# Kernel tuning notes

Hardware: AMD Instinct MI355X
Metric: run time of the kernel (lower is better)

## Reference

```python
import jax, jax.numpy as jnp
import numpy as np

B, T, D, H = 8192, 128, 16, 32
EPS = 1e-5  # BatchNorm1d default eps (eval mode, running stats)


def setup_inputs() -> dict:
    key = jax.random.key(0)
    ks = iter(jax.random.split(key, 64))

    def nrm(shape, s=0.1):
        return jax.random.normal(next(ks), shape, jnp.float32) * s

    inp = {}
    inp["S"] = nrm((B, T, D), 1.0)
    inp["g_S"] = nrm((B, T), 1.0)
    inp["times"] = jnp.linspace(0.0, 1.0, T, dtype=jnp.float32)
    inp["payoff_T"] = nrm((B,), 1.0)
    inp["delta_T"] = nrm((B, D), 1.0)
    # init_hidden: uniform(-0.1, 0.1), shape [num_layers=2, B, H]
    inp["h_price0"] = jax.random.uniform(next(ks), (2, B, H), jnp.float32, -0.1, 0.1)
    inp["h_delta0"] = jax.random.uniform(next(ks), (2, B, H), jnp.float32, -0.1, 0.1)
    # params for price net (prefix p_, out_dim=1) and delta net (prefix d_, out_dim=D)
    for pfx, out_dim in (("p", 1), ("d", D)):
        inp[pfx + "_Wih0"] = nrm((3 * H, 2 * D))
        inp[pfx + "_Whh0"] = nrm((3 * H, H))
        inp[pfx + "_bih0"] = nrm((3 * H,))
        inp[pfx + "_bhh0"] = nrm((3 * H,))
        inp[pfx + "_Wih1"] = nrm((3 * H, H))
        inp[pfx + "_Whh1"] = nrm((3 * H, H))
        inp[pfx + "_bih1"] = nrm((3 * H,))
        inp[pfx + "_bhh1"] = nrm((3 * H,))
        inp[pfx + "_embW"] = nrm((H, H))
        inp[pfx + "_embB"] = nrm((H,))
        inp[pfx + "_bng"] = jnp.ones((H,), jnp.float32)
        inp[pfx + "_bnb"] = jnp.zeros((H,), jnp.float32)
        inp[pfx + "_bnm"] = nrm((H,))
        inp[pfx + "_bnv"] = jax.random.uniform(next(ks), (H,), jnp.float32, 0.5, 1.5)
        inp[pfx + "_outW"] = nrm((out_dim, H))
        inp[pfx + "_outB"] = nrm((out_dim,))
    return inp


def _gru_cell(x, h, Wih, Whh, bih, bhh):
    # PyTorch GRU cell, gate order (r, z, n)
    gi = x @ Wih.T + bih
    gh = h @ Whh.T + bhh
    ir, iz, inn = jnp.split(gi, 3, axis=-1)
    hr, hz, hn = jnp.split(gh, 3, axis=-1)
    r = jax.nn.sigmoid(ir + hr)
    z = jax.nn.sigmoid(iz + hz)
    n = jnp.tanh(inn + r * hn)
    return (1.0 - z) * n + z * h


def _head(y, Wemb, bemb, g, b, m, v, Wout, bout, sig):
    # Linear -> BatchNorm1d (eval, running stats) -> SiLU -> Linear [-> Sigmoid]
    e = y @ Wemb.T + bemb
    e = (e - m) * jax.lax.rsqrt(v + EPS) * g + b
    e = e * jax.nn.sigmoid(e)  # SiLU
    o = e @ Wout.T + bout
    return jax.nn.sigmoid(o) if sig else o


def reference(S, g_S, times, payoff_T, delta_T, h_price0, h_delta0,
              p_Wih0, p_Whh0, p_bih0, p_bhh0, p_Wih1, p_Whh1, p_bih1, p_bhh1,
              p_embW, p_embB, p_bng, p_bnb, p_bnm, p_bnv, p_outW, p_outB,
              d_Wih0, d_Whh0, d_bih0, d_bhh0, d_Wih1, d_Whh1, d_bih1, d_bhh1,
              d_embW, d_embB, d_bng, d_bnb, d_bnm, d_bnv, d_outW, d_outB):
    # X = cat([S, g_S expanded to d]) -> [B, T, 2D]
    gS = jnp.broadcast_to(g_S[..., None], S.shape)
    X = jnp.concatenate([S, gS], axis=-1)
    Xr = jnp.swapaxes(X, 0, 1)[::-1]  # [T, B, 2D], time reversed (loop goes t=T-1..0)

    def step(carry, xt):
        hp0, hp1, hd0, hd1 = carry
        hp0 = _gru_cell(xt, hp0, p_Wih0, p_Whh0, p_bih0, p_bhh0)
        hp1 = _gru_cell(hp0, hp1, p_Wih1, p_Whh1, p_bih1, p_bhh1)
        hd0 = _gru_cell(xt, hd0, d_Wih0, d_Whh0, d_bih0, d_bhh0)
        hd1 = _gru_cell(hd0, hd1, d_Wih1, d_Whh1, d_bih1, d_bhh1)
        return (hp0, hp1, hd0, hd1), (hp1, hd1)

    carry0 = (h_price0[0], h_price0[1], h_delta0[0], h_delta0[1])
    _, (Yp, Yd) = jax.lax.scan(step, carry0, Xr)
    # flip time back to forward order: outputs were collected for t=T-1..0
    Yp = jnp.swapaxes(Yp[::-1], 0, 1)  # [B, T, H]
    Yd = jnp.swapaxes(Yd[::-1], 0, 1)  # [B, T, H]
    prices = _head(Yp, p_embW, p_embB, p_bng, p_bnb, p_bnm, p_bnv, p_outW, p_outB, False)  # [B,T,1]
    deltas = _head(Yd, d_embW, d_embB, d_bng, d_bnb, d_bnm, d_bnv, d_outW, d_outB, True)   # [B,T,D]
    return (prices, deltas)
```

## Files before the change

### kernel.cpp

```cpp
#include <hip/hip_runtime.h>
#include <hip/hip_bf16.h>
#include <stdint.h>

#define DI __device__ __forceinline__

typedef float f32x4 __attribute__((ext_vector_type(4)));
typedef short bf16x8 __attribute__((ext_vector_type(8)));

constexpr int BB = 8192, TT = 128, DD = 16, HH = 32;
constexpr float kEPS = 1e-5f;
constexpr float kLOG2E = 1.44269504088896340736f;

DI float rcpf_(float x) { return __builtin_amdgcn_rcpf(x); }
DI float exp2f_(float x) { return __builtin_amdgcn_exp2f(x); }
DI float sigm(float x) { return rcpf_(1.0f + exp2f_(-kLOG2E * x)); }

DI uint32_t cvtpk(float lo, float hi) {
  uint32_t r;
  asm("v_cvt_pk_bf16_f32 %0, %1, %2" : "=v"(r) : "v"(lo), "v"(hi));
  return r;
}

DI f32x4 mfma_(bf16x8 a, bf16x8 b, f32x4 c) {
  return __builtin_amdgcn_mfma_f32_16x16x32_bf16(a, b, c, 0, 0, 0);
}

union U4 { uint4 q; bf16x8 v; uint32_t u[4]; };

__global__ void prep_net(const float* Wih0, const float* Whh0,
                         const float* bih0, const float* bhh0,
                         const float* Wih1, const float* Whh1,
                         const float* bih1, const float* bhh1,
                         const float* embW, const float* embB,
                         const float* bng, const float* bnb,
                         const float* bnm, const float* bnv,
                         const float* outW, const float* outB,
                         int outDim, uint8_t* wsbase) {
  int tid = threadIdx.x;
  uint16_t* W = (uint16_t*)wsbase;
  float* bias = (float*)(wsbase + 27648);
  auto cvt = [](float f) -> uint16_t {
    union { float f; uint32_t u; } v; v.f = f;
    uint32_t u = v.u;
    return (uint16_t)((u + 0x7FFF + ((u >> 16) & 1)) >> 16);
  };
  for (int idx = tid; idx < 27 * 64; idx += 256) {
    int tile = idx >> 6, l = idx & 63, cc = l & 15, gg = l >> 4;
    uint16_t* dst = W + (size_t)idx * 8;
    if (tile < 24) {
      const float* mats[4] = {Wih0, Whh0, Wih1, Whh1};
      const float* src = mats[tile / 6];
      int sub = tile % 6;
      int row = sub * 16 + cc;
      float sc = (sub < 4) ? -kLOG2E : 2.0f * kLOG2E;
#pragma unroll
      for (int j = 0; j < 8; ++j) {
        int k = (j < 4) ? 4 * gg + j : 16 + 4 * gg + (j - 4);
        dst[j] = cvt(src[row * 32 + k] * sc);
      }
    } else if (tile < 26) {
      int row = (tile - 24) * 16 + cc;
      float a = bng[row] * rsqrtf(bnv[row] + kEPS);
#pragma unroll
      for (int j = 0; j < 8; ++j) {
        int k = (j < 4) ? 4 * gg + j : 16 + 4 * gg + (j - 4);
        dst[j] = cvt(embW[row * 32 + k] * a);
      }
    } else {
      int rrow = (cc < outDim) ? cc : 0;
      float sc = (cc < outDim) ? 1.0f : 0.0f;
#pragma unroll
      for (int j = 0; j < 8; ++j) {
        int k = (j < 4) ? 4 * gg + j : 16 + 4 * gg + (j - 4);
        dst[j] = cvt(outW[rrow * 32 + k] * sc);
      }
    }
  }
  for (int idx = tid; idx < 304; idx += 256) {
    int tile = idx >> 4, n = idx & 15;
    float v;
    if (tile < 8) {
      if (tile < 4)      v = (bih0[tile * 16 + n] + bhh0[tile * 16 + n]) * (-kLOG2E);
      else if (tile < 6) v = bih0[64 + (tile - 4) * 16 + n] * (2.0f * kLOG2E);
      else               v = bhh0[64 + (tile - 6) * 16 + n] * (2.0f * kLOG2E);
    } else if (tile < 16) {
      int tt = tile - 8;
      if (tt < 4)        v = (bih1[tt * 16 + n] + bhh1[tt * 16 + n]) * (-kLOG2E);
      else if (tt < 6)   v = bih1[64 + (tt - 4) * 16 + n] * (2.0f * kLOG2E);
      else               v = bhh1[64 + (tt - 6) * 16 + n] * (2.0f * kLOG2E);
    } else if (tile < 18) {
      int nn = (tile - 16) * 16 + n;
      float a = bng[nn] * rsqrtf(bnv[nn] + kEPS);
      v = a * (embB[nn] - bnm[nn]) + bnb[nn];
    } else {
      v = (n < outDim) ? outB[n] : 0.0f;
    }
    bias[idx] = v;
  }
}

__global__ __launch_bounds__(128, 2) void rnn_fused(
    const float* __restrict__ S, const float* __restrict__ gS,
    const float* __restrict__ hp0, const float* __restrict__ hd0,
    const uint8_t* __restrict__ ws, float* __restrict__ out) {
  const int tid = threadIdx.x, lane = tid & 63, wid = tid >> 6;
  const int net = blockIdx.x & 1;
  const int b0 = (blockIdx.x >> 1) * 16;
  const int c = lane & 15, g = lane >> 4;

  const uint16_t* W = (const uint16_t*)(ws + net * 32768);
  const float* bias = (const float*)(ws + net * 32768 + 27648);
  const float* hsrc = net ? hd0 : hp0;

  __shared__ uint4 ring0[8][64];
  __shared__ volatile int flags[2];
  if (tid < 2) flags[tid] = 0;
  __syncthreads();

  auto waitGE = [&](int idx, int target) {
    if (flags[idx] >= target) return;
    do { __builtin_amdgcn_s_sleep(1); } while (flags[idx] < target);
  };

  auto packB = [&](const float (&v)[8]) -> bf16x8 {
    U4 t;
    t.u[0] = cvtpk(v[0], v[1]); t.u[1] = cvtpk(v[2], v[3]);
    t.u[2] = cvtpk(v[4], v[5]); t.u[3] = cvtpk(v[6], v[7]);
    return t.v;
  };

  auto gruStep = [&](const bf16x8 (&Wi)[6], const bf16x8 (&Wh)[6],
                     const f32x4 (&Bb)[8], bf16x8 xf, bf16x8 hf,
                     float (&hC)[8]) {
    f32x4 r0 = mfma_(Wi[0], xf, Bb[0]); r0 = mfma_(Wh[0], hf, r0);
    f32x4 r1 = mfma_(Wi[1], xf, Bb[1]); r1 = mfma_(Wh[1], hf, r1);
    f32x4 z0 = mfma_(Wi[2], xf, Bb[2]); z0 = mfma_(Wh[2], hf, z0);
    f32x4 z1 = mfma_(Wi[3], xf, Bb[3]); z1 = mfma_(Wh[3], hf, z1);
    f32x4 ni0 = mfma_(Wi[4], xf, Bb[4]);
    f32x4 ni1 = mfma_(Wi[5], xf, Bb[5]);
    f32x4 nh0 = mfma_(Wh[4], hf, Bb[6]);
    f32x4 nh1 = mfma_(Wh[5], hf, Bb[7]);
#pragma unroll
    for (int r = 0; r < 4; ++r) {
      float rg0 = rcpf_(1.0f + exp2f_(r0[r]));
      float rg1 = rcpf_(1.0f + exp2f_(r1[r]));
      float w0 = ni0[r] + rg0 * nh0[r];
      float w1 = ni1[r] + rg1 * nh1[r];
      float En0 = exp2f_(w0), En1 = exp2f_(w1);
      float Ez0 = exp2f_(z0[r]), Ez1 = exp2f_(z1[r]);
      float hv0 = hC[r], hv1 = hC[4 + r];
      float num0 = (hv0 - Ez0) + En0 * (hv0 + Ez0);
      float num1 = (hv1 - Ez1) + En1 * (hv1 + Ez1);
      float den0 = (1.0f + En0) * (1.0f + Ez0);
      float den1 = (1.0f + En1) * (1.0f + Ez1);
      hC[r]     = num0 * rcpf_(den0);
      hC[4 + r] = num1 * rcpf_(den1);
    }
  };

  auto loadState = [&](const float* row, float (&hC)[8]) -> bf16x8 {
    f32x4 a = *(const f32x4*)(row + 4 * g);
    f32x4 b = *(const f32x4*)(row + 16 + 4 * g);
#pragma unroll
    for (int r = 0; r < 4; ++r) { hC[r] = a[r]; hC[4 + r] = b[r]; }
    U4 t;
    t.u[0] = cvtpk(a[0], a[1]); t.u[1] = cvtpk(a[2], a[3]);
    t.u[2] = cvtpk(b[0], b[1]); t.u[3] = cvtpk(b[2], b[3]);
    return t.v;
  };

  if (wid == 0) {
    bf16x8 Wi[6], Wh[6];
#pragma unroll
    for (int t = 0; t < 6; ++t) {
      Wi[t] = *(const bf16x8*)(W + ((0 + t) * 64 + lane) * 8);
      Wh[t] = *(const bf16x8*)(W + ((6 + t) * 64 + lane) * 8);
    }
    f32x4 Bb[8];
#pragma unroll
    for (int t = 0; t < 8; ++t)
      Bb[t] = *(const f32x4*)(bias + t * 16 + 4 * g);

    float h0C[8];
    bf16x8 h0B = loadState(hsrc + (size_t)(b0 + c) * HH, h0C);

    auto mkX = [&](f32x4 sv, float gsv) -> bf16x8 {
      uint32_t pkg = cvtpk(gsv, gsv);
      U4 t;
      t.u[0] = cvtpk(sv[0], sv[1]);
      t.u[1] = cvtpk(sv[2], sv[3]);
      t.u[2] = pkg;
      t.u[3] = pkg;
      return t.v;
    };

    const float* Sbase  = S  + (size_t)(b0 + c) * TT * DD + 4 * g;
    const float* gSbase = gS + (size_t)(b0 + c) * TT;

    f32x4 sv0 = *(const f32x4*)(Sbase + (size_t)(TT - 1) * DD);
    float gv0 = gSbase[TT - 1];
    f32x4 sv1 = *(const f32x4*)(Sbase + (size_t)(TT - 2) * DD);
    float gv1 = gSbase[TT - 2];

#pragma unroll 2
    for (int i = 0; i < TT; ++i) {
      int tn = TT - 3 - i; if (tn < 0) tn = 0;
      f32x4 svn = *(const f32x4*)(Sbase + (size_t)tn * DD);
      float gvn = gSbase[tn];

      bf16x8 xB = mkX(sv0, gv0);
      gruStep(Wi, Wh, Bb, xB, h0B, h0C);
      h0B = packB(h0C);

      if (i >= 8 && (i & 3) == 0) waitGE(1, i - 4);
      asm volatile("" ::: "memory");
      { U4 u; u.v = h0B; ring0[i & 7][lane] = u.q; }
      if ((i & 3) == 3) {
        asm volatile("s_waitcnt lgkmcnt(0)" ::: "memory");
        if (lane == 0) flags[0] = i + 1;
      }

      sv0 = sv1; gv0 = gv1;
      sv1 = svn; gv1 = gvn;
    }
  } else {
    bf16x8 Wi[6], Wh[6], We0, We1, Wo;
#pragma unroll
    for (int t = 0; t < 6; ++t) {
      Wi[t] = *(const bf16x8*)(W + ((12 + t) * 64 + lane) * 8);
      Wh[t] = *(const bf16x8*)(W + ((18 + t) * 64 + lane) * 8);
    }
    We0 = *(const bf16x8*)(W + (24 * 64 + lane) * 8);
    We1 = *(const bf16x8*)(W + (25 * 64 + lane) * 8);
    Wo  = *(const bf16x8*)(W + (26 * 64 + lane) * 8);
    f32x4 Bb[8];
#pragma unroll
    for (int t = 0; t < 8; ++t)
      Bb[t] = *(const f32x4*)(bias + (8 + t) * 16 + 4 * g);
    const f32x4 Be0 = *(const f32x4*)(bias + 16 * 16 + 4 * g);
    const f32x4 Be1 = *(const f32x4*)(bias + 17 * 16 + 4 * g);
    const f32x4 Bo  = *(const f32x4*)(bias + 18 * 16 + 4 * g);

    float h1C[8];
    bf16x8 h1B = loadState(hsrc + ((size_t)BB + b0 + c) * HH, h1C);

    auto head = [&](bf16x8 h1f, int th) {
      f32x4 e0 = mfma_(We0, h1f, Be0);
      f32x4 e1 = mfma_(We1, h1f, Be1);
      float es[8];
#pragma unroll
      for (int r = 0; r < 4; ++r) {
        float a = e0[r], b = e1[r];
        es[r]     = a * sigm(a);
        es[4 + r] = b * sigm(b);
      }
      bf16x8 ef = packB(es);
      f32x4 o = mfma_(Wo, ef, Bo);
      if (net == 0) {
        if (lane < 16) out[(size_t)(b0 + c) * TT + th] = o[0];
      } else {
        f32x4 so;
#pragma unroll
        for (int r = 0; r < 4; ++r) so[r] = sigm(o[r]);
        *(f32x4*)(out + (size_t)BB * TT +
                  ((size_t)(b0 + c) * TT + th) * DD + 4 * g) = so;
      }
    };

#pragma unroll 1
    for (int i = 0; i < TT; ++i) {
      if ((i & 3) == 0) waitGE(0, i + 4);
      asm volatile("" ::: "memory");
      U4 u; u.q = ring0[i & 7][lane];
      asm volatile("s_waitcnt lgkmcnt(0)" ::: "memory");
      if ((i & 3) == 3 && lane == 0) flags[1] = i + 1;

      bf16x8 h1prev = h1B;
      gruStep(Wi, Wh, Bb, u.v, h1B, h1C);
      if (i > 0) head(h1prev, TT - i);
      h1B = packB(h1C);
    }
    head(h1B, 0);
  }
}

extern "C" void kernel_launch(void* const* d_in, const int* in_sizes, int n_in,
                              void* d_out, int out_size, void* d_ws,
                              size_t ws_size, hipStream_t stream) {
  const float* S   = (const float*)d_in[0];
  const float* gS  = (const float*)d_in[1];
  const float* hp0 = (const float*)d_in[5];
  const float* hd0 = (const float*)d_in[6];
  uint8_t* ws = (uint8_t*)d_ws;

  prep_net<<<1, 256, 0, stream>>>(
      (const float*)d_in[7],  (const float*)d_in[8],  (const float*)d_in[9],
      (const float*)d_in[10], (const float*)d_in[11], (const float*)d_in[12],
      (const float*)d_in[13], (const float*)d_in[14], (const float*)d_in[15],
      (const float*)d_in[16], (const float*)d_in[17], (const float*)d_in[18],
      (const float*)d_in[19], (const float*)d_in[20], (const float*)d_in[21],
      (const float*)d_in[22], 1, ws);
  prep_net<<<1, 256, 0, stream>>>(
      (const float*)d_in[23], (const float*)d_in[24], (const float*)d_in[25],
      (const float*)d_in[26], (const float*)d_in[27], (const float*)d_in[28],
      (const float*)d_in[29], (const float*)d_in[30], (const float*)d_in[31],
      (const float*)d_in[32], (const float*)d_in[33], (const float*)d_in[34],
      (const float*)d_in[35], (const float*)d_in[36], (const float*)d_in[37],
      (const float*)d_in[38], 16, ws + 32768);

  rnn_fused<<<dim3((BB / 16) * 2), dim3(128), 0, stream>>>(S, gS, hp0, hd0,
                                                           ws, (float*)d_out);
}
```

Before: 151.4 us.

## Split layer-1 GRU and output head into separate warps with second ring

Adds a third wavefront per block so that the layer-0 GRU, the layer-1 GRU and the embedding/output head each run on their own wave, connected by LDS ring buffers and flag handshakes. The head work moves off the layer-1 recurrence critical path. Each wave now processes two timesteps per loop iteration with one flag update, which cuts synchronisation frequency. The cost is more threads per block, an extra ring buffer and tighter occupancy, since launch bounds change to 192 threads with 3 blocks per CU.

```diff
diff --git a/kernel.cpp b/kernel.cpp
--- a/kernel.cpp
+++ b/kernel.cpp
@@ -99,7 +99,7 @@
   }
 }
 
-__global__ __launch_bounds__(128, 2) void rnn_fused(
+__global__ __launch_bounds__(192, 3) void rnn_fused(
     const float* __restrict__ S, const float* __restrict__ gS,
     const float* __restrict__ hp0, const float* __restrict__ hd0,
     const uint8_t* __restrict__ ws, float* __restrict__ out) {
@@ -113,8 +113,9 @@
   const float* hsrc = net ? hd0 : hp0;
 
   __shared__ uint4 ring0[8][64];
-  __shared__ volatile int flags[2];
-  if (tid < 2) flags[tid] = 0;
+  __shared__ uint4 ring1[8][64];
+  __shared__ volatile int flags[4];
+  if (tid < 4) flags[tid] = 0;
   __syncthreads();
 
   auto waitGE = [&](int idx, int target) {
@@ -196,53 +197,87 @@
 
     const float* Sbase  = S  + (size_t)(b0 + c) * TT * DD + 4 * g;
     const float* gSbase = gS + (size_t)(b0 + c) * TT;
-
-    f32x4 sv0 = *(const f32x4*)(Sbase + (size_t)(TT - 1) * DD);
-    float gv0 = gSbase[TT - 1];
-    f32x4 sv1 = *(const f32x4*)(Sbase + (size_t)(TT - 2) * DD);
-    float gv1 = gSbase[TT - 2];
-
-#pragma unroll 2
-    for (int i = 0; i < TT; ++i) {
-      int tn = TT - 3 - i; if (tn < 0) tn = 0;
-      f32x4 svn = *(const f32x4*)(Sbase + (size_t)tn * DD);
-      float gvn = gSbase[tn];
-
-      bf16x8 xB = mkX(sv0, gv0);
-      gruStep(Wi, Wh, Bb, xB, h0B, h0C);
+    auto loadX = [&](int t, f32x4& a, float& gv) {
+      a = *(const f32x4*)(Sbase + (size_t)t * DD); gv = gSbase[t];
+    };
+
+    f32x4 ca0, ca1, na0, na1;
+    float cg0, cg1, ng0, ng1;
+    loadX(TT - 1, ca0, cg0);
+    loadX(TT - 2, ca1, cg1);
+
+#pragma unroll 1
+    for (int ip = 0; ip < TT / 2; ++ip) {
+      int tn0 = TT - 3 - 2 * ip; if (tn0 < 0) tn0 = 0;
+      int tn1 = TT - 4 - 2 * ip; if (tn1 < 0) tn1 = 0;
+      loadX(tn0, na0, ng0);
+      loadX(tn1, na1, ng1);
+
+      bf16x8 x0 = mkX(ca0, cg0);
+      gruStep(Wi, Wh, Bb, x0, h0B, h0C);
       h0B = packB(h0C);
-
-      if (i >= 8 && (i & 3) == 0) waitGE(1, i - 4);
+      U4 f0v; f0v.v = h0B;
+      bf16x8 x1 = mkX(ca1, cg1);
+      gruStep(Wi, Wh, Bb, x1, h0B, h0C);
+      h0B = packB(h0C);
+      U4 f1v; f1v.v = h0B;
+
+      if (ip >= 4) waitGE(1, 2 * ip - 6);
       asm volatile("" ::: "memory");
-      { U4 u; u.v = h0B; ring0[i & 7][lane] = u.q; }
-      if ((i & 3) == 3) {
-        asm volatile("s_waitcnt lgkmcnt(0)" ::: "memory");
-        if (lane == 0) flags[0] = i + 1;
-      }
-
-      sv0 = sv1; gv0 = gv1;
-      sv1 = svn; gv1 = gvn;
-    }
-  } else {
-    bf16x8 Wi[6], Wh[6], We0, We1, Wo;
+      ring0[(2 * ip) & 7][lane]     = f0v.q;
+      ring0[(2 * ip + 1) & 7][lane] = f1v.q;
+      asm volatile("s_waitcnt lgkmcnt(0)" ::: "memory");
+      if (lane == 0) flags[0] = 2 * ip + 2;
+
+      ca0 = na0; cg0 = ng0;
+      ca1 = na1; cg1 = ng1;
+    }
+  } else if (wid == 1) {
+    bf16x8 Wi[6], Wh[6];
 #pragma unroll
     for (int t = 0; t < 6; ++t) {
       Wi[t] = *(const bf16x8*)(W + ((12 + t) * 64 + lane) * 8);
       Wh[t] = *(const bf16x8*)(W + ((18 + t) * 64 + lane) * 8);
     }
-    We0 = *(const bf16x8*)(W + (24 * 64 + lane) * 8);
-    We1 = *(const bf16x8*)(W + (25 * 64 + lane) * 8);
-    Wo  = *(const bf16x8*)(W + (26 * 64 + lane) * 8);
     f32x4 Bb[8];
 #pragma unroll
     for (int t = 0; t < 8; ++t)
       Bb[t] = *(const f32x4*)(bias + (8 + t) * 16 + 4 * g);
+
+    float h1C[8];
+    bf16x8 h1B = loadState(hsrc + ((size_t)BB + b0 + c) * HH, h1C);
+
+#pragma unroll 1
+    for (int ip = 0; ip < TT / 2; ++ip) {
+      waitGE(0, 2 * ip + 2);
+      asm volatile("" ::: "memory");
+      U4 u0, u1;
+      u0.q = ring0[(2 * ip) & 7][lane];
+      u1.q = ring0[(2 * ip + 1) & 7][lane];
+      asm volatile("s_waitcnt lgkmcnt(0)" ::: "memory");
+      if (lane == 0) flags[1] = 2 * ip + 2;
+
+      gruStep(Wi, Wh, Bb, u0.v, h1B, h1C);
+      h1B = packB(h1C);
+      U4 f0v; f0v.v = h1B;
+      gruStep(Wi, Wh, Bb, u1.v, h1B, h1C);
+      h1B = packB(h1C);
+      U4 f1v; f1v.v = h1B;
+
+      if (ip >= 4) waitGE(3, 2 * ip - 6);
+      asm volatile("" ::: "memory");
+      ring1[(2 * ip) & 7][lane]     = f0v.q;
+      ring1[(2 * ip + 1) & 7][lane] = f1v.q;
+      asm volatile("s_waitcnt lgkmcnt(0)" ::: "memory");
+      if (lane == 0) flags[2] = 2 * ip + 2;
+    }
+  } else {
+    bf16x8 We0 = *(const bf16x8*)(W + (24 * 64 + lane) * 8);
+    bf16x8 We1 = *(const bf16x8*)(W + (25 * 64 + lane) * 8);
+    bf16x8 Wo  = *(const bf16x8*)(W + (26 * 64 + lane) * 8);
     const f32x4 Be0 = *(const f32x4*)(bias + 16 * 16 + 4 * g);
     const f32x4 Be1 = *(const f32x4*)(bias + 17 * 16 + 4 * g);
     const f32x4 Bo  = *(const f32x4*)(bias + 18 * 16 + 4 * g);
-
-    float h1C[8];
-    bf16x8 h1B = loadState(hsrc + ((size_t)BB + b0 + c) * HH, h1C);
 
     auto head = [&](bf16x8 h1f, int th) {
       f32x4 e0 = mfma_(We0, h1f, Be0);
@@ -268,19 +303,18 @@
     };
 
 #pragma unroll 1
-    for (int i = 0; i < TT; ++i) {
-      if ((i & 3) == 0) waitGE(0, i + 4);
+    for (int ip = 0; ip < TT / 2; ++ip) {
+      waitGE(2, 2 * ip + 2);
       asm volatile("" ::: "memory");
-      U4 u; u.q = ring0[i & 7][lane];
+      U4 u0, u1;
+      u0.q = ring1[(2 * ip) & 7][lane];
+      u1.q = ring1[(2 * ip + 1) & 7][lane];
       asm volatile("s_waitcnt lgkmcnt(0)" ::: "memory");
-      if ((i & 3) == 3 && lane == 0) flags[1] = i + 1;
-
-      bf16x8 h1prev = h1B;
-      gruStep(Wi, Wh, Bb, u.v, h1B, h1C);
-      if (i > 0) head(h1prev, TT - i);
-      h1B = packB(h1C);
-    }
-    head(h1B, 0);
+      if (lane == 0) flags[3] = 2 * ip + 2;
+
+      head(u0.v, TT - 1 - 2 * ip);
+      head(u1.v, TT - 2 - 2 * ip);
+    }
   }
 }
 
@@ -308,6 +342,6 @@
       (const float*)d_in[35], (const float*)d_in[36], (const float*)d_in[37],
       (const float*)d_in[38], 16, ws + 32768);
 
-  rnn_fused<<<dim3((BB / 16) * 2), dim3(128), 0, stream>>>(S, gS, hp0, hd0,
+  rnn_fused<<<dim3((BB / 16) * 2), dim3(192), 0, stream>>>(S, gS, hp0, hd0,
                                                            ws, (float*)d_out);
 }
```

Result: slower. 158.5 us (+4.7%).

## Merge two-wave GRU layer pipeline into a single wave with skewed layer interleaving

Applied to the files above, without the earlier changes.

Replaces the producer/consumer split, where one wave ran GRU layer 0 and another ran layer 1 plus the head through an LDS ring buffer and spin flags, with a single 64-thread wave per block. That wave holds all weights in registers and interleaves layer 1 at step t with layer 0 at step t-1, which gives independent work for ILP. This removes LDS traffic, flag polling and block synchronisation, but doubles the serial work per wave, halves the threads per block and raises register pressure. It also folds the -log2e scale into the delta output weights so the output sigmoid drops one multiply, and packs the gate math into float2 vectors.

```diff
diff --git a/kernel.cpp b/kernel.cpp
--- a/kernel.cpp
+++ b/kernel.cpp
@@ -5,6 +5,7 @@
 #define DI __device__ __forceinline__
 
 typedef float f32x4 __attribute__((ext_vector_type(4)));
+typedef float f32x2 __attribute__((ext_vector_type(2)));
 typedef short bf16x8 __attribute__((ext_vector_type(8)));
 
 constexpr int BB = 8192, TT = 128, DD = 16, HH = 32;
@@ -44,6 +45,7 @@
     uint32_t u = v.u;
     return (uint16_t)((u + 0x7FFF + ((u >> 16) & 1)) >> 16);
   };
+  const float oscale = (outDim == 16) ? -kLOG2E : 1.0f;
   for (int idx = tid; idx < 27 * 64; idx += 256) {
     int tile = idx >> 6, l = idx & 63, cc = l & 15, gg = l >> 4;
     uint16_t* dst = W + (size_t)idx * 8;
@@ -68,7 +70,7 @@
       }
     } else {
       int rrow = (cc < outDim) ? cc : 0;
-      float sc = (cc < outDim) ? 1.0f : 0.0f;
+      float sc = (cc < outDim) ? oscale : 0.0f;
 #pragma unroll
       for (int j = 0; j < 8; ++j) {
         int k = (j < 4) ? 4 * gg + j : 16 + 4 * gg + (j - 4);
@@ -93,17 +95,17 @@
       float a = bng[nn] * rsqrtf(bnv[nn] + kEPS);
       v = a * (embB[nn] - bnm[nn]) + bnb[nn];
     } else {
-      v = (n < outDim) ? outB[n] : 0.0f;
+      v = (n < outDim) ? outB[n] * oscale : 0.0f;
     }
     bias[idx] = v;
   }
 }
 
-__global__ __launch_bounds__(128, 2) void rnn_fused(
+__global__ __launch_bounds__(64, 1) void rnn_fused(
     const float* __restrict__ S, const float* __restrict__ gS,
     const float* __restrict__ hp0, const float* __restrict__ hd0,
     const uint8_t* __restrict__ ws, float* __restrict__ out) {
-  const int tid = threadIdx.x, lane = tid & 63, wid = tid >> 6;
+  const int lane = threadIdx.x & 63;
   const int net = blockIdx.x & 1;
   const int b0 = (blockIdx.x >> 1) * 16;
   const int c = lane & 15, g = lane >> 4;
@@ -112,15 +114,14 @@
   const float* bias = (const float*)(ws + net * 32768 + 27648);
   const float* hsrc = net ? hd0 : hp0;
 
-  __shared__ uint4 ring0[8][64];
-  __shared__ volatile int flags[2];
-  if (tid < 2) flags[tid] = 0;
-  __syncthreads();
-
-  auto waitGE = [&](int idx, int target) {
-    if (flags[idx] >= target) return;
-    do { __builtin_amdgcn_s_sleep(1); } while (flags[idx] < target);
-  };
+  bf16x8 Wt[27];
+#pragma unroll
+  for (int t = 0; t < 27; ++t)
+    Wt[t] = *(const bf16x8*)(W + (t * 64 + lane) * 8);
+  f32x4 Bq[19];
+#pragma unroll
+  for (int t = 0; t < 19; ++t)
+    Bq[t] = *(const f32x4*)(bias + t * 16 + 4 * g);
 
   auto packB = [&](const float (&v)[8]) -> bf16x8 {
     U4 t;
@@ -129,32 +130,35 @@
     return t.v;
   };
 
-  auto gruStep = [&](const bf16x8 (&Wi)[6], const bf16x8 (&Wh)[6],
-                     const f32x4 (&Bb)[8], bf16x8 xf, bf16x8 hf,
+  auto gruStep = [&](int wih, int whh, int bb, bf16x8 xf, bf16x8 hf,
                      float (&hC)[8]) {
-    f32x4 r0 = mfma_(Wi[0], xf, Bb[0]); r0 = mfma_(Wh[0], hf, r0);
-    f32x4 r1 = mfma_(Wi[1], xf, Bb[1]); r1 = mfma_(Wh[1], hf, r1);
-    f32x4 z0 = mfma_(Wi[2], xf, Bb[2]); z0 = mfma_(Wh[2], hf, z0);
-    f32x4 z1 = mfma_(Wi[3], xf, Bb[3]); z1 = mfma_(Wh[3], hf, z1);
-    f32x4 ni0 = mfma_(Wi[4], xf, Bb[4]);
-    f32x4 ni1 = mfma_(Wi[5], xf, Bb[5]);
-    f32x4 nh0 = mfma_(Wh[4], hf, Bb[6]);
-    f32x4 nh1 = mfma_(Wh[5], hf, Bb[7]);
+    f32x4 r0 = mfma_(Wt[wih + 0], xf, Bq[bb + 0]); r0 = mfma_(Wt[whh + 0], hf, r0);
+    f32x4 r1 = mfma_(Wt[wih + 1], xf, Bq[bb + 1]); r1 = mfma_(Wt[whh + 1], hf, r1);
+    f32x4 z0 = mfma_(Wt[wih + 2], xf, Bq[bb + 2]); z0 = mfma_(Wt[whh + 2], hf, z0);
+    f32x4 z1 = mfma_(Wt[wih + 3], xf, Bq[bb + 3]); z1 = mfma_(Wt[whh + 3], hf, z1);
+    f32x4 ni0 = mfma_(Wt[wih + 4], xf, Bq[bb + 4]);
+    f32x4 ni1 = mfma_(Wt[wih + 5], xf, Bq[bb + 5]);
+    f32x4 nh0 = mfma_(Wt[whh + 4], hf, Bq[bb + 6]);
+    f32x4 nh1 = mfma_(Wt[whh + 5], hf, Bq[bb + 7]);
+    const f32x2 one = {1.0f, 1.0f};
 #pragma unroll
     for (int r = 0; r < 4; ++r) {
-      float rg0 = rcpf_(1.0f + exp2f_(r0[r]));
-      float rg1 = rcpf_(1.0f + exp2f_(r1[r]));
-      float w0 = ni0[r] + rg0 * nh0[r];
-      float w1 = ni1[r] + rg1 * nh1[r];
-      float En0 = exp2f_(w0), En1 = exp2f_(w1);
-      float Ez0 = exp2f_(z0[r]), Ez1 = exp2f_(z1[r]);
-      float hv0 = hC[r], hv1 = hC[4 + r];
-      float num0 = (hv0 - Ez0) + En0 * (hv0 + Ez0);
-      float num1 = (hv1 - Ez1) + En1 * (hv1 + Ez1);
-      float den0 = (1.0f + En0) * (1.0f + Ez0);
-      float den1 = (1.0f + En1) * (1.0f + Ez1);
-      hC[r]     = num0 * rcpf_(den0);
-      hC[4 + r] = num1 * rcpf_(den1);
+      f32x2 ra = {r0[r], r1[r]};
+      f32x2 za = {z0[r], z1[r]};
+      f32x2 ni = {ni0[r], ni1[r]};
+      f32x2 nh = {nh0[r], nh1[r]};
+      f32x2 hv = {hC[r], hC[4 + r]};
+      f32x2 era = {exp2f_(ra[0]), exp2f_(ra[1])};
+      f32x2 t1 = one + era;
+      f32x2 rg = {rcpf_(t1[0]), rcpf_(t1[1])};
+      f32x2 w = ni + rg * nh;
+      f32x2 En = {exp2f_(w[0]), exp2f_(w[1])};
+      f32x2 Ez = {exp2f_(za[0]), exp2f_(za[1])};
+      f32x2 num = (hv - Ez) + En * (hv + Ez);
+      f32x2 den = (one + En) * (one + Ez);
+      f32x2 rd = {rcpf_(den[0]), rcpf_(den[1])};
+      f32x2 res = num * rd;
+      hC[r] = res[0]; hC[4 + r] = res[1];
     }
   };
 
@@ -169,119 +173,73 @@
     return t.v;
   };
 
-  if (wid == 0) {
-    bf16x8 Wi[6], Wh[6];
-#pragma unroll
-    for (int t = 0; t < 6; ++t) {
-      Wi[t] = *(const bf16x8*)(W + ((0 + t) * 64 + lane) * 8);
-      Wh[t] = *(const bf16x8*)(W + ((6 + t) * 64 + lane) * 8);
-    }
-    f32x4 Bb[8];
-#pragma unroll
-    for (int t = 0; t < 8; ++t)
-      Bb[t] = *(const f32x4*)(bias + t * 16 + 4 * g);
-
-    float h0C[8];
-    bf16x8 h0B = loadState(hsrc + (size_t)(b0 + c) * HH, h0C);
-
-    auto mkX = [&](f32x4 sv, float gsv) -> bf16x8 {
-      uint32_t pkg = cvtpk(gsv, gsv);
-      U4 t;
-      t.u[0] = cvtpk(sv[0], sv[1]);
-      t.u[1] = cvtpk(sv[2], sv[3]);
-      t.u[2] = pkg;
-      t.u[3] = pkg;
-      return t.v;
-    };
-
-    const float* Sbase  = S  + (size_t)(b0 + c) * TT * DD + 4 * g;
-    const float* gSbase = gS + (size_t)(b0 + c) * TT;
-
-    f32x4 sv0 = *(const f32x4*)(Sbase + (size_t)(TT - 1) * DD);
-    float gv0 = gSbase[TT - 1];
-    f32x4 sv1 = *(const f32x4*)(Sbase + (size_t)(TT - 2) * DD);
-    float gv1 = gSbase[TT - 2];
-
-#pragma unroll 2
-    for (int i = 0; i < TT; ++i) {
-      int tn = TT - 3 - i; if (tn < 0) tn = 0;
-      f32x4 svn = *(const f32x4*)(Sbase + (size_t)tn * DD);
-      float gvn = gSbase[tn];
-
-      bf16x8 xB = mkX(sv0, gv0);
-      gruStep(Wi, Wh, Bb, xB, h0B, h0C);
-      h0B = packB(h0C);
-
-      if (i >= 8 && (i & 3) == 0) waitGE(1, i - 4);
-      asm volatile("" ::: "memory");
-      { U4 u; u.v = h0B; ring0[i & 7][lane] = u.q; }
-      if ((i & 3) == 3) {
-        asm volatile("s_waitcnt lgkmcnt(0)" ::: "memory");
-        if (lane == 0) flags[0] = i + 1;
-      }
-
-      sv0 = sv1; gv0 = gv1;
-      sv1 = svn; gv1 = gvn;
-    }
-  } else {
-    bf16x8 Wi[6], Wh[6], We0, We1, Wo;
-#pragma unroll
-    for (int t = 0; t < 6; ++t) {
-      Wi[t] = *(const bf16x8*)(W + ((12 + t) * 64 + lane) * 8);
-      Wh[t] = *(const bf16x8*)(W + ((18 + t) * 64 + lane) * 8);
-    }
-    We0 = *(const bf16x8*)(W + (24 * 64 + lane) * 8);
-    We1 = *(const bf16x8*)(W + (25 * 64 + lane) * 8);
-    Wo  = *(const bf16x8*)(W + (26 * 64 + lane) * 8);
-    f32x4 Bb[8];
-#pragma unroll
-    for (int t = 0; t < 8; ++t)
-      Bb[t] = *(const f32x4*)(bias + (8 + t) * 16 + 4 * g);
-    const f32x4 Be0 = *(const f32x4*)(bias + 16 * 16 + 4 * g);
-    const f32x4 Be1 = *(const f32x4*)(bias + 17 * 16 + 4 * g);
-    const f32x4 Bo  = *(const f32x4*)(bias + 18 * 16 + 4 * g);
-
-    float h1C[8];
-    bf16x8 h1B = loadState(hsrc + ((size_t)BB + b0 + c) * HH, h1C);
-
-    auto head = [&](bf16x8 h1f, int th) {
-      f32x4 e0 = mfma_(We0, h1f, Be0);
-      f32x4 e1 = mfma_(We1, h1f, Be1);
-      float es[8];
-#pragma unroll
-      for (int r = 0; r < 4; ++r) {
-        float a = e0[r], b = e1[r];
-        es[r]     = a * sigm(a);
-        es[4 + r] = b * sigm(b);
-      }
-      bf16x8 ef = packB(es);
-      f32x4 o = mfma_(Wo, ef, Bo);
-      if (net == 0) {
-        if (lane < 16) out[(size_t)(b0 + c) * TT + th] = o[0];
-      } else {
-        f32x4 so;
-#pragma unroll
-        for (int r = 0; r < 4; ++r) so[r] = sigm(o[r]);
-        *(f32x4*)(out + (size_t)BB * TT +
-                  ((size_t)(b0 + c) * TT + th) * DD + 4 * g) = so;
-      }
-    };
+  auto mkX = [&](f32x4 sv, float gsv) -> bf16x8 {
+    uint32_t pkg = cvtpk(gsv, gsv);
+    U4 t;
+    t.u[0] = cvtpk(sv[0], sv[1]);
+    t.u[1] = cvtpk(sv[2], sv[3]);
+    t.u[2] = pkg;
+    t.u[3] = pkg;
+    return t.v;
+  };
+
+  auto head = [&](bf16x8 h1f, int th) {
+    f32x4 e0 = mfma_(Wt[24], h1f, Bq[16]);
+    f32x4 e1 = mfma_(Wt[25], h1f, Bq[17]);
+    float es[8];
+#pragma unroll
+    for (int r = 0; r < 4; ++r) {
+      float a = e0[r], b = e1[r];
+      es[r]     = a * sigm(a);
+      es[4 + r] = b * sigm(b);
+    }
+    bf16x8 ef = packB(es);
+    f32x4 o = mfma_(Wt[26], ef, Bq[18]);
+    if (net == 0) {
+      if (lane < 16) out[(size_t)(b0 + c) * TT + th] = o[0];
+    } else {
+      f32x4 so;
+#pragma unroll
+      for (int r = 0; r < 4; ++r) so[r] = rcpf_(1.0f + exp2f_(o[r]));
+      *(f32x4*)(out + (size_t)BB * TT +
+                ((size_t)(b0 + c) * TT + th) * DD + 4 * g) = so;
+    }
+  };
+
+  float h0C[8], h1C[8];
+  bf16x8 h0B = loadState(hsrc + (size_t)(b0 + c) * HH, h0C);
+  bf16x8 h1B = loadState(hsrc + ((size_t)BB + b0 + c) * HH, h1C);
+
+  const float* Sbase  = S  + (size_t)(b0 + c) * TT * DD + 4 * g;
+  const float* gSbase = gS + (size_t)(b0 + c) * TT;
+
+  f32x4 xa = *(const f32x4*)(Sbase + (size_t)(TT - 1) * DD);
+  float ga = gSbase[TT - 1];
+  f32x4 xb = *(const f32x4*)(Sbase + (size_t)(TT - 2) * DD);
+  float gb = gSbase[TT - 2];
+
+  bf16x8 xB = mkX(xa, ga);
+  gruStep(0, 6, 0, xB, h0B, h0C);
+  h0B = packB(h0C);
 
 #pragma unroll 1
-    for (int i = 0; i < TT; ++i) {
-      if ((i & 3) == 0) waitGE(0, i + 4);
-      asm volatile("" ::: "memory");
-      U4 u; u.q = ring0[i & 7][lane];
-      asm volatile("s_waitcnt lgkmcnt(0)" ::: "memory");
-      if ((i & 3) == 3 && lane == 0) flags[1] = i + 1;
-
-      bf16x8 h1prev = h1B;
-      gruStep(Wi, Wh, Bb, u.v, h1B, h1C);
-      if (i > 0) head(h1prev, TT - i);
-      h1B = packB(h1C);
-    }
-    head(h1B, 0);
+  for (int t = TT - 2; t >= 0; --t) {
+    xB = mkX(xb, gb);
+    int tn = (t > 0) ? t - 1 : 0;
+    xa = *(const f32x4*)(Sbase + (size_t)tn * DD);
+    ga = gSbase[tn];
+
+    gruStep(12, 18, 8, h0B, h1B, h1C);
+    gruStep(0, 6, 0, xB, h0B, h0C);
+    h1B = packB(h1C);
+    h0B = packB(h0C);
+    head(h1B, t + 1);
+
+    xb = xa; gb = ga;
   }
+  gruStep(12, 18, 8, h0B, h1B, h1C);
+  h1B = packB(h1C);
+  head(h1B, 0);
 }
 
 extern "C" void kernel_launch(void* const* d_in, const int* in_sizes, int n_in,
@@ -308,6 +266,6 @@
       (const float*)d_in[35], (const float*)d_in[36], (const float*)d_in[37],
       (const float*)d_in[38], 16, ws + 32768);
 
-  rnn_fused<<<dim3((BB / 16) * 2), dim3(128), 0, stream>>>(S, gS, hp0, hd0,
-                                                           ws, (float*)d_out);
-}
+  rnn_fused<<<dim3((BB / 16) * 2), dim3(64), 0, stream>>>(S, gS, hp0, hd0,
+                                                          ws, (float*)d_out);
+}
```

Measured after the change: 158.9 us. 1.05x slower.
